# Performance work log

Hardware: AMD Instinct MI355X
Metric: run time of the kernel (lower is better)

The kernel has to match this reference:

```python
import jax, jax.numpy as jnp
import numpy as np

D = 1024

def setup_inputs() -> dict:
    key = jax.random.key(0)
    ks = jax.random.split(key, 9)
    s = 1.0 / np.sqrt(D)
    return {
        "x": jax.random.normal(ks[0], (4, 2048, D), dtype=jnp.float32),
        "y": jax.random.normal(ks[1], (4, 2048, D), dtype=jnp.float32),
        "z": jax.random.normal(ks[2], (4, 2048, D), dtype=jnp.float32),
        "Wq": jax.random.uniform(ks[3], (D, D), jnp.float32, -s, s),
        "bq": jax.random.uniform(ks[4], (D,), jnp.float32, -s, s),
        "Wk": jax.random.uniform(ks[5], (D, D), jnp.float32, -s, s),
        "bk": jax.random.uniform(ks[6], (D,), jnp.float32, -s, s),
        "Wv": jax.random.uniform(ks[7], (D, D), jnp.float32, -s, s),
        "bv": jax.random.uniform(ks[8], (D,), jnp.float32, -s, s),
    }

def reference(x, y, z, Wq, bq, Wk, bk, Wv, bv):
    # nn.Linear: x @ W^T + b
    Q = jnp.einsum('bsd,ed->bse', x, Wq) + bq  # [B,S,D]
    K = jnp.einsum('bsd,ed->bse', y, Wk) + bk
    V = jnp.einsum('bsd,ed->bse', z, Wv) + bv
    scores = jnp.einsum('bqd,bkd->bqk', Q, K) / jnp.sqrt(jnp.float32(Q.shape[-1]))
    weights = jax.nn.softmax(scores, axis=-1)  # [B,S,S]
    return jnp.einsum('bqk,bkd->bqd', weights, V)
```

## Files before the change

kernel.cpp:

```cpp
#include <hip/hip_runtime.h>
#include <hip/hip_bf16.h>

typedef unsigned short u16;
typedef __bf16 bf16x8 __attribute__((ext_vector_type(8)));
typedef float  f32x4  __attribute__((ext_vector_type(4)));
typedef u16    u16x8  __attribute__((ext_vector_type(8)));

__device__ __forceinline__ u16 f2bf(float f) {
    unsigned u = __float_as_uint(f);
    u = (u + 0x7fffu + ((u >> 16) & 1u)) >> 16;
    return (u16)u;
}
__device__ __forceinline__ float bf2f(u16 h) {
    return __uint_as_float(((unsigned)h) << 16);
}

__global__ __launch_bounds__(256) void cvt_bf16_kernel(
    const float* __restrict__ src, u16* __restrict__ dst, int n8)
{
    int i = blockIdx.x * 256 + threadIdx.x;
    if (i >= n8) return;
    const float4* s4 = (const float4*)src;
    float4 a = s4[2 * i], b = s4[2 * i + 1];
    u16x8 o;
    o[0] = f2bf(a.x); o[1] = f2bf(a.y); o[2] = f2bf(a.z); o[3] = f2bf(a.w);
    o[4] = f2bf(b.x); o[5] = f2bf(b.y); o[6] = f2bf(b.z); o[7] = f2bf(b.w);
    ((u16x8*)dst)[i] = o;
}

#define BMM 256
#define BNN 128
#define BKK 64
#define BUFU 24576
#define LDSB (3 * BUFU * 2)

__device__ __forceinline__ void gload_lds16(const void* g, void* l) {
    __builtin_amdgcn_global_load_lds(
        (__attribute__((address_space(1))) void*)g,
        (__attribute__((address_space(3))) void*)l, 16, 0, 0);
}

template<bool OUT_BF16, bool HAS_BIAS>
__global__ __launch_bounds__(512, 2) void gemm8p(
    const u16* __restrict__ A, const u16* __restrict__ Bm,
    const float* __restrict__ bias, void* __restrict__ C,
    int M, int N, int K, float scale,
    long long aBS, long long bBS, long long cBS)
{
    extern __shared__ u16 lds[];
    A  += (size_t)blockIdx.z * aBS;
    Bm += (size_t)blockIdx.z * bBS;

    const int m0 = blockIdx.y * BMM;
    const int n0 = blockIdx.x * BNN;
    const int tid  = threadIdx.x;
    const int lane = tid & 63;
    const int wave = tid >> 6;
    const int wm   = wave >> 2;
    const int wn   = wave & 3;
    const int fr   = lane & 15;
    const int kg   = lane >> 4;

    const int sl_a = lane >> 3;
    const int swsl = (lane & 7) ^ sl_a;
    const u16* gAs = A  + (size_t)(m0 + wave * 8 + sl_a) * K + swsl * 8;
    const u16* gBs = Bm + (size_t)(n0 + wave * 8 + sl_a) * K + swsl * 8;
    const int ldsW = wave * 512;

    auto stageA = [&](u16* wbase, size_t gc, int i) {
        gload_lds16(gAs + gc + (size_t)i * 64 * K, wbase + i * 4096 + ldsW);
    };
    auto stageB = [&](u16* wbase, size_t gc, int i) {
        gload_lds16(gBs + gc + (size_t)i * 64 * K, wbase + 16384 + i * 4096 + ldsW);
    };

    f32x4 acc[8][2] = {};

    const int NT = K / BKK;
    const int swz = fr & 7;

    {
        u16* b0 = lds;
        u16* b1 = lds + BUFU;
        #pragma unroll
        for (int i = 0; i < 4; ++i) stageA(b0, 0, i);
        #pragma unroll
        for (int i = 0; i < 2; ++i) stageB(b0, 0, i);
        #pragma unroll
        for (int i = 0; i < 4; ++i) stageA(b1, BKK, i);
        #pragma unroll
        for (int i = 0; i < 2; ++i) stageB(b1, BKK, i);
        asm volatile("s_waitcnt vmcnt(6)" ::: "memory");
        __builtin_amdgcn_s_barrier();
    }

    int br = 0, bw = 2;
    for (int t = 0; t < NT; ++t) {
        const u16* sa = lds + br * BUFU;
        const u16* sb = sa + 16384;
        u16* wbase = lds + bw * BUFU;
        const bool st = (t + 2 < NT);
        const size_t gc = (size_t)(t + 2) * BKK;

        bf16x8 bF[2][2];
        #pragma unroll
        for (int n = 0; n < 2; ++n)
            #pragma unroll
            for (int ks = 0; ks < 2; ++ks)
                bF[n][ks] = *(const bf16x8*)&sb[(wn * 32 + n * 16 + fr) * 64
                                + ((((ks << 2) | kg) ^ swz) << 3)];
        bf16x8 aF0[4][2];
        #pragma unroll
        for (int m = 0; m < 4; ++m)
            #pragma unroll
            for (int ks = 0; ks < 2; ++ks)
                aF0[m][ks] = *(const bf16x8*)&sa[(wm * 128 + m * 16 + fr) * 64
                                + ((((ks << 2) | kg) ^ swz) << 3)];
        if (st) { stageA(wbase, gc, 0); stageA(wbase, gc, 1); stageB(wbase, gc, 0); }
        __builtin_amdgcn_s_barrier();
        __builtin_amdgcn_s_setprio(1);
        #pragma unroll
        for (int m = 0; m < 4; ++m)
            #pragma unroll
            for (int n = 0; n < 2; ++n)
                #pragma unroll
                for (int ks = 0; ks < 2; ++ks)
                    acc[m][n] = __builtin_amdgcn_mfma_f32_16x16x32_bf16(
                        aF0[m][ks], bF[n][ks], acc[m][n], 0, 0, 0);
        __builtin_amdgcn_s_setprio(0);
        __builtin_amdgcn_s_barrier();

        bf16x8 aF1[4][2];
        #pragma unroll
        for (int m = 0; m < 4; ++m)
            #pragma unroll
            for (int ks = 0; ks < 2; ++ks)
                aF1[m][ks] = *(const bf16x8*)&sa[(wm * 128 + 64 + m * 16 + fr) * 64
                                + ((((ks << 2) | kg) ^ swz) << 3)];
        if (st) { stageA(wbase, gc, 2); stageA(wbase, gc, 3); stageB(wbase, gc, 1); }
        if (st) asm volatile("s_waitcnt vmcnt(6)" ::: "memory");
        else    asm volatile("s_waitcnt vmcnt(0)" ::: "memory");
        __builtin_amdgcn_s_barrier();
        __builtin_amdgcn_s_setprio(1);
        #pragma unroll
        for (int m = 0; m < 4; ++m)
            #pragma unroll
            for (int n = 0; n < 2; ++n)
                #pragma unroll
                for (int ks = 0; ks < 2; ++ks)
                    acc[4 + m][n] = __builtin_amdgcn_mfma_f32_16x16x32_bf16(
                        aF1[m][ks], bF[n][ks], acc[4 + m][n], 0, 0, 0);
        __builtin_amdgcn_s_setprio(0);
        __builtin_amdgcn_s_barrier();

        br = (br == 2) ? 0 : br + 1;
        bw = (bw == 2) ? 0 : bw + 1;
    }

    if (OUT_BF16) {
        u16* Cb = (u16*)C + (size_t)blockIdx.z * cBS;
        #pragma unroll
        for (int mi = 0; mi < 8; ++mi) {
            const int row0 = m0 + wm * 128 + mi * 16 + kg * 4;
            #pragma unroll
            for (int n = 0; n < 2; ++n) {
                const int col = n0 + wn * 32 + n * 16 + fr;
                const float badd = HAS_BIAS ? bias[col] : 0.0f;
                f32x4 v = acc[mi][n];
                #pragma unroll
                for (int q = 0; q < 4; ++q)
                    Cb[(size_t)(row0 + q) * N + col] = f2bf(v[q] * scale + badd);
            }
        }
    } else {
        float* Cf = (float*)C + (size_t)blockIdx.z * cBS;
        #pragma unroll
        for (int mi = 0; mi < 8; ++mi) {
            const int row0 = m0 + wm * 128 + mi * 16 + kg * 4;
            #pragma unroll
            for (int n = 0; n < 2; ++n) {
                const int col = n0 + wn * 32 + n * 16 + fr;
                const float badd = HAS_BIAS ? bias[col] : 0.0f;
                f32x4 v = acc[mi][n];
                #pragma unroll
                for (int q = 0; q < 4; ++q)
                    Cf[(size_t)(row0 + q) * N + col] = v[q] * scale + badd;
            }
        }
    }
}

__global__ __launch_bounds__(256) void transpose_bf16(
    const u16* __restrict__ V, u16* __restrict__ Vt)
{
    __shared__ u16 tile[64][72];
    const int b  = blockIdx.z;
    const int k0 = blockIdx.y * 64;
    const int d0 = blockIdx.x * 64;
    const int tr = threadIdx.x >> 3;
    const int tc = (threadIdx.x & 7) * 8;

    const u16* src = V + ((size_t)b * 2048 + k0) * 1024 + d0;
    #pragma unroll
    for (int i = 0; i < 2; ++i) {
        int r = tr + i * 32;
        *(u16x8*)&tile[r][tc] = *(const u16x8*)&src[(size_t)r * 1024 + tc];
    }
    __syncthreads();
    u16* dst = Vt + ((size_t)b * 1024 + d0) * 2048 + k0;
    #pragma unroll
    for (int i = 0; i < 2; ++i) {
        int r = tr + i * 32;
        u16x8 o;
        #pragma unroll
        for (int j = 0; j < 8; ++j) o[j] = tile[tc + j][r];
        *(u16x8*)&dst[(size_t)r * 2048 + tc] = o;
    }
}

__global__ __launch_bounds__(256) void softmax_kernel(u16* __restrict__ SP)
{
    const size_t row = blockIdx.x;
    u16x8* rp = (u16x8*)(SP + row * 2048);
    const int tid  = threadIdx.x;
    const int lane = tid & 63;
    const int wv   = tid >> 6;

    u16x8 v = rp[tid];
    float f[8];
    #pragma unroll
    for (int j = 0; j < 8; ++j) f[j] = bf2f(v[j]);

    float m = f[0];
    #pragma unroll
    for (int j = 1; j < 8; ++j) m = fmaxf(m, f[j]);
    #pragma unroll
    for (int o = 32; o; o >>= 1) m = fmaxf(m, __shfl_xor(m, o, 64));

    __shared__ float red[8];
    if (lane == 0) red[wv] = m;
    __syncthreads();
    m = fmaxf(fmaxf(red[0], red[1]), fmaxf(red[2], red[3]));

    float e[8], s = 0.f;
    #pragma unroll
    for (int j = 0; j < 8; ++j) { e[j] = __expf(f[j] - m); s += e[j]; }
    #pragma unroll
    for (int o = 32; o; o >>= 1) s += __shfl_xor(s, o, 64);
    if (lane == 0) red[4 + wv] = s;
    __syncthreads();
    s = (red[4] + red[5]) + (red[6] + red[7]);
    const float inv = 1.0f / s;

    u16x8 o8;
    #pragma unroll
    for (int j = 0; j < 8; ++j) o8[j] = f2bf(e[j] * inv);
    rp[tid] = o8;
}

extern "C" void kernel_launch(void* const* d_in, const int* in_sizes, int n_in,
                              void* d_out, int out_size, void* d_ws, size_t ws_size,
                              hipStream_t stream)
{
    const int Bn = 4, S = 2048, D = 1024;
    const size_t nx = (size_t)Bn * S * D;
    const size_t nw = (size_t)D * D;

    const float* x  = (const float*)d_in[0];
    const float* y  = (const float*)d_in[1];
    const float* z  = (const float*)d_in[2];
    const float* Wq = (const float*)d_in[3];
    const float* bq = (const float*)d_in[4];
    const float* Wk = (const float*)d_in[5];
    const float* bk = (const float*)d_in[6];
    const float* Wv = (const float*)d_in[7];
    const float* bv = (const float*)d_in[8];

    u16* xb  = (u16*)d_ws;
    u16* yb  = xb + nx;
    u16* zb  = yb + nx;
    u16* wqb = zb + nx;
    u16* wkb = wqb + nw;
    u16* wvb = wkb + nw;
    u16* Qb  = wvb + nw;
    u16* Kb  = Qb + nx;
    u16* Vb  = Kb + nx;
    u16* Vt  = Vb + nx;
    u16* Pb  = xb;

    hipFuncSetAttribute((const void*)gemm8p<true,  true >,
                        hipFuncAttributeMaxDynamicSharedMemorySize, LDSB);
    hipFuncSetAttribute((const void*)gemm8p<true,  false>,
                        hipFuncAttributeMaxDynamicSharedMemorySize, LDSB);
    hipFuncSetAttribute((const void*)gemm8p<false, false>,
                        hipFuncAttributeMaxDynamicSharedMemorySize, LDSB);

    const int n8x = (int)(nx / 8), n8w = (int)(nw / 8);
    cvt_bf16_kernel<<<(n8x + 255) / 256, 256, 0, stream>>>(x, xb, n8x);
    cvt_bf16_kernel<<<(n8x + 255) / 256, 256, 0, stream>>>(y, yb, n8x);
    cvt_bf16_kernel<<<(n8x + 255) / 256, 256, 0, stream>>>(z, zb, n8x);
    cvt_bf16_kernel<<<(n8w + 255) / 256, 256, 0, stream>>>(Wq, wqb, n8w);
    cvt_bf16_kernel<<<(n8w + 255) / 256, 256, 0, stream>>>(Wk, wkb, n8w);
    cvt_bf16_kernel<<<(n8w + 255) / 256, 256, 0, stream>>>(Wv, wvb, n8w);

    dim3 gQKV(D / BNN, (Bn * S) / BMM, 1);
    gemm8p<true, true><<<gQKV, 512, LDSB, stream>>>(xb, wqb, bq, Qb, Bn * S, D, D, 1.0f, 0, 0, 0);
    gemm8p<true, true><<<gQKV, 512, LDSB, stream>>>(yb, wkb, bk, Kb, Bn * S, D, D, 1.0f, 0, 0, 0);
    gemm8p<true, true><<<gQKV, 512, LDSB, stream>>>(zb, wvb, bv, Vb, Bn * S, D, D, 1.0f, 0, 0, 0);

    transpose_bf16<<<dim3(D / 64, S / 64, Bn), 256, 0, stream>>>(Vb, Vt);

    gemm8p<true, false><<<dim3(S / BNN, S / BMM, Bn), 512, LDSB, stream>>>(
        Qb, Kb, nullptr, Pb, S, S, D, 0.03125f,
        (long long)S * D, (long long)S * D, (long long)S * S);

    softmax_kernel<<<Bn * S, 256, 0, stream>>>(Pb);

    gemm8p<false, false><<<dim3(D / BNN, S / BMM, Bn), 512, LDSB, stream>>>(
        Pb, Vt, nullptr, d_out, S, D, S, 1.0f,
        (long long)S * S, (long long)D * S, (long long)S * D);
}
```

Before: 352.0 us.

## Reshape wave tiles to 64x64 and software-pipeline LDS fragment reads with fewer barriers

Each of the eight waves in the GEMM now computes a square 64x64 sub-tile in a 4x2 wave grid, replacing the 128x32 sub-tile in a 2x4 grid. Each MFMA batch then needs the same number of A and B fragment reads. The k-loop splits into two k-halves. The fragments for the next half are read from LDS while the current half's MFMAs run. All global-to-LDS staging for stage t+2 is issued at once, and only one barrier per iteration remains instead of four. The aim is more fragment reuse per LDS read and less synchronisation stall, at the cost of a hand-scheduled pipeline that relies on the waitcnt and barrier placement being exactly right.

```diff
diff --git a/kernel.cpp b/kernel.cpp
--- a/kernel.cpp
+++ b/kernel.cpp
@@ -28,11 +28,8 @@
     ((u16x8*)dst)[i] = o;
 }
 
-#define BMM 256
-#define BNN 128
-#define BKK 64
-#define BUFU 24576
-#define LDSB (3 * BUFU * 2)
+#define BUF_N 24576
+#define LDS_N (3 * BUF_N * 2)
 
 __device__ __forceinline__ void gload_lds16(const void* g, void* l) {
     __builtin_amdgcn_global_load_lds(
@@ -41,7 +38,7 @@
 }
 
 template<bool OUT_BF16, bool HAS_BIAS>
-__global__ __launch_bounds__(512, 2) void gemm8p(
+__global__ __launch_bounds__(512, 2) void gemm_p(
     const u16* __restrict__ A, const u16* __restrict__ Bm,
     const float* __restrict__ bias, void* __restrict__ C,
     int M, int N, int K, float scale,
@@ -51,122 +48,120 @@
     A  += (size_t)blockIdx.z * aBS;
     Bm += (size_t)blockIdx.z * bBS;
 
-    const int m0 = blockIdx.y * BMM;
-    const int n0 = blockIdx.x * BNN;
+    const int m0 = blockIdx.y * 256;
+    const int n0 = blockIdx.x * 128;
     const int tid  = threadIdx.x;
     const int lane = tid & 63;
     const int wave = tid >> 6;
-    const int wm   = wave >> 2;
-    const int wn   = wave & 3;
+    const int wm   = wave >> 1;
+    const int wn   = wave & 1;
     const int fr   = lane & 15;
     const int kg   = lane >> 4;
 
-    const int sl_a = lane >> 3;
-    const int swsl = (lane & 7) ^ sl_a;
-    const u16* gAs = A  + (size_t)(m0 + wave * 8 + sl_a) * K + swsl * 8;
-    const u16* gBs = Bm + (size_t)(n0 + wave * 8 + sl_a) * K + swsl * 8;
+    const int rl  = tid >> 3;
+    const int sw8 = ((tid & 7) ^ (rl & 7)) * 8;
+    const u16* gA = A  + (size_t)(m0 + rl) * K + sw8;
+    const u16* gB = Bm + (size_t)(n0 + rl) * K + sw8;
     const int ldsW = wave * 512;
 
-    auto stageA = [&](u16* wbase, size_t gc, int i) {
-        gload_lds16(gAs + gc + (size_t)i * 64 * K, wbase + i * 4096 + ldsW);
+    auto stA = [&](u16* bufb, int tk, int c) {
+        gload_lds16(gA + (size_t)c * 64 * K + (size_t)tk * 64,
+                    bufb + c * 4096 + ldsW);
     };
-    auto stageB = [&](u16* wbase, size_t gc, int i) {
-        gload_lds16(gBs + gc + (size_t)i * 64 * K, wbase + 16384 + i * 4096 + ldsW);
+    auto stB = [&](u16* bufb, int tk, int c) {
+        gload_lds16(gB + (size_t)c * 64 * K + (size_t)tk * 64,
+                    bufb + 16384 + c * 4096 + ldsW);
     };
 
-    f32x4 acc[8][2] = {};
-
-    const int NT = K / BKK;
-    const int swz = fr & 7;
-
-    {
-        u16* b0 = lds;
-        u16* b1 = lds + BUFU;
-        #pragma unroll
-        for (int i = 0; i < 4; ++i) stageA(b0, 0, i);
-        #pragma unroll
-        for (int i = 0; i < 2; ++i) stageB(b0, 0, i);
-        #pragma unroll
-        for (int i = 0; i < 4; ++i) stageA(b1, BKK, i);
-        #pragma unroll
-        for (int i = 0; i < 2; ++i) stageB(b1, BKK, i);
-        asm volatile("s_waitcnt vmcnt(6)" ::: "memory");
-        __builtin_amdgcn_s_barrier();
-    }
-
-    int br = 0, bw = 2;
+    auto rdA = [&](const u16* sa, int m, int ks) {
+        return *(const bf16x8*)&sa[(wm * 64 + m * 16 + fr) * 64
+                                   + ((((ks << 2) | kg) ^ (fr & 7)) << 3)];
+    };
+    auto rdB = [&](const u16* sb, int n, int ks) {
+        return *(const bf16x8*)&sb[(wn * 64 + n * 16 + fr) * 64
+                                   + ((((ks << 2) | kg) ^ (fr & 7)) << 3)];
+    };
+
+    f32x4 acc[4][4] = {};
+    bf16x8 a0[4], b0[4], a1[4], b1[4];
+    const int NT = K / 64;
+
+    u16 *p0 = lds, *p1 = lds + BUF_N, *p2 = lds + 2 * BUF_N;
+
+    #pragma unroll
+    for (int c = 0; c < 4; ++c) stA(p0, 0, c);
+    #pragma unroll
+    for (int c = 0; c < 2; ++c) stB(p0, 0, c);
+    #pragma unroll
+    for (int c = 0; c < 4; ++c) stA(p1, 1, c);
+    #pragma unroll
+    for (int c = 0; c < 2; ++c) stB(p1, 1, c);
+    asm volatile("s_waitcnt vmcnt(6)" ::: "memory");
+    __builtin_amdgcn_s_barrier();
+
+    #pragma unroll
+    for (int m = 0; m < 4; ++m) a0[m] = rdA(p0, m, 0);
+    #pragma unroll
+    for (int n = 0; n < 4; ++n) b0[n] = rdB(p0 + 16384, n, 0);
+
     for (int t = 0; t < NT; ++t) {
-        const u16* sa = lds + br * BUFU;
-        const u16* sb = sa + 16384;
-        u16* wbase = lds + bw * BUFU;
+        const u16* sa = p0;
+        const u16* sb = p0 + 16384;
         const bool st = (t + 2 < NT);
-        const size_t gc = (size_t)(t + 2) * BKK;
-
-        bf16x8 bF[2][2];
-        #pragma unroll
-        for (int n = 0; n < 2; ++n)
-            #pragma unroll
-            for (int ks = 0; ks < 2; ++ks)
-                bF[n][ks] = *(const bf16x8*)&sb[(wn * 32 + n * 16 + fr) * 64
-                                + ((((ks << 2) | kg) ^ swz) << 3)];
-        bf16x8 aF0[4][2];
+
+        #pragma unroll
+        for (int m = 0; m < 4; ++m) a1[m] = rdA(sa, m, 1);
+        #pragma unroll
+        for (int n = 0; n < 4; ++n) b1[n] = rdB(sb, n, 1);
+        if (st) {
+            #pragma unroll
+            for (int c = 0; c < 4; ++c) stA(p2, t + 2, c);
+            #pragma unroll
+            for (int c = 0; c < 2; ++c) stB(p2, t + 2, c);
+        }
+        __builtin_amdgcn_s_setprio(1);
         #pragma unroll
         for (int m = 0; m < 4; ++m)
             #pragma unroll
-            for (int ks = 0; ks < 2; ++ks)
-                aF0[m][ks] = *(const bf16x8*)&sa[(wm * 128 + m * 16 + fr) * 64
-                                + ((((ks << 2) | kg) ^ swz) << 3)];
-        if (st) { stageA(wbase, gc, 0); stageA(wbase, gc, 1); stageB(wbase, gc, 0); }
-        __builtin_amdgcn_s_barrier();
-        __builtin_amdgcn_s_setprio(1);
-        #pragma unroll
-        for (int m = 0; m < 4; ++m)
-            #pragma unroll
-            for (int n = 0; n < 2; ++n)
-                #pragma unroll
-                for (int ks = 0; ks < 2; ++ks)
-                    acc[m][n] = __builtin_amdgcn_mfma_f32_16x16x32_bf16(
-                        aF0[m][ks], bF[n][ks], acc[m][n], 0, 0, 0);
+            for (int n = 0; n < 4; ++n)
+                acc[m][n] = __builtin_amdgcn_mfma_f32_16x16x32_bf16(
+                    a0[m], b0[n], acc[m][n], 0, 0, 0);
         __builtin_amdgcn_s_setprio(0);
-        __builtin_amdgcn_s_barrier();
-
-        bf16x8 aF1[4][2];
-        #pragma unroll
-        for (int m = 0; m < 4; ++m)
-            #pragma unroll
-            for (int ks = 0; ks < 2; ++ks)
-                aF1[m][ks] = *(const bf16x8*)&sa[(wm * 128 + 64 + m * 16 + fr) * 64
-                                + ((((ks << 2) | kg) ^ swz) << 3)];
-        if (st) { stageA(wbase, gc, 2); stageA(wbase, gc, 3); stageB(wbase, gc, 1); }
+
+        asm volatile("s_waitcnt lgkmcnt(0)" ::: "memory");
         if (st) asm volatile("s_waitcnt vmcnt(6)" ::: "memory");
         else    asm volatile("s_waitcnt vmcnt(0)" ::: "memory");
         __builtin_amdgcn_s_barrier();
+        if (t + 1 < NT) {
+            const u16* na = p1;
+            const u16* nb = p1 + 16384;
+            #pragma unroll
+            for (int m = 0; m < 4; ++m) a0[m] = rdA(na, m, 0);
+            #pragma unroll
+            for (int n = 0; n < 4; ++n) b0[n] = rdB(nb, n, 0);
+        }
         __builtin_amdgcn_s_setprio(1);
         #pragma unroll
         for (int m = 0; m < 4; ++m)
             #pragma unroll
-            for (int n = 0; n < 2; ++n)
-                #pragma unroll
-                for (int ks = 0; ks < 2; ++ks)
-                    acc[4 + m][n] = __builtin_amdgcn_mfma_f32_16x16x32_bf16(
-                        aF1[m][ks], bF[n][ks], acc[4 + m][n], 0, 0, 0);
+            for (int n = 0; n < 4; ++n)
+                acc[m][n] = __builtin_amdgcn_mfma_f32_16x16x32_bf16(
+                    a1[m], b1[n], acc[m][n], 0, 0, 0);
         __builtin_amdgcn_s_setprio(0);
-        __builtin_amdgcn_s_barrier();
-
-        br = (br == 2) ? 0 : br + 1;
-        bw = (bw == 2) ? 0 : bw + 1;
+
+        u16* tmp = p0; p0 = p1; p1 = p2; p2 = tmp;
     }
 
     if (OUT_BF16) {
         u16* Cb = (u16*)C + (size_t)blockIdx.z * cBS;
         #pragma unroll
-        for (int mi = 0; mi < 8; ++mi) {
-            const int row0 = m0 + wm * 128 + mi * 16 + kg * 4;
-            #pragma unroll
-            for (int n = 0; n < 2; ++n) {
-                const int col = n0 + wn * 32 + n * 16 + fr;
+        for (int m = 0; m < 4; ++m) {
+            const int row0 = m0 + wm * 64 + m * 16 + kg * 4;
+            #pragma unroll
+            for (int n = 0; n < 4; ++n) {
+                const int col = n0 + wn * 64 + n * 16 + fr;
                 const float badd = HAS_BIAS ? bias[col] : 0.0f;
-                f32x4 v = acc[mi][n];
+                f32x4 v = acc[m][n];
                 #pragma unroll
                 for (int q = 0; q < 4; ++q)
                     Cb[(size_t)(row0 + q) * N + col] = f2bf(v[q] * scale + badd);
@@ -175,13 +170,13 @@
     } else {
         float* Cf = (float*)C + (size_t)blockIdx.z * cBS;
         #pragma unroll
-        for (int mi = 0; mi < 8; ++mi) {
-            const int row0 = m0 + wm * 128 + mi * 16 + kg * 4;
-            #pragma unroll
-            for (int n = 0; n < 2; ++n) {
-                const int col = n0 + wn * 32 + n * 16 + fr;
+        for (int m = 0; m < 4; ++m) {
+            const int row0 = m0 + wm * 64 + m * 16 + kg * 4;
+            #pragma unroll
+            for (int n = 0; n < 4; ++n) {
+                const int col = n0 + wn * 64 + n * 16 + fr;
                 const float badd = HAS_BIAS ? bias[col] : 0.0f;
-                f32x4 v = acc[mi][n];
+                f32x4 v = acc[m][n];
                 #pragma unroll
                 for (int q = 0; q < 4; ++q)
                     Cf[(size_t)(row0 + q) * N + col] = v[q] * scale + badd;
@@ -288,12 +283,12 @@
     u16* Vt  = Vb + nx;
     u16* Pb  = xb;
 
-    hipFuncSetAttribute((const void*)gemm8p<true,  true >,
-                        hipFuncAttributeMaxDynamicSharedMemorySize, LDSB);
-    hipFuncSetAttribute((const void*)gemm8p<true,  false>,
-                        hipFuncAttributeMaxDynamicSharedMemorySize, LDSB);
-    hipFuncSetAttribute((const void*)gemm8p<false, false>,
-                        hipFuncAttributeMaxDynamicSharedMemorySize, LDSB);
+    hipFuncSetAttribute((const void*)gemm_p<true,  true >,
+                        hipFuncAttributeMaxDynamicSharedMemorySize, LDS_N);
+    hipFuncSetAttribute((const void*)gemm_p<true,  false>,
+                        hipFuncAttributeMaxDynamicSharedMemorySize, LDS_N);
+    hipFuncSetAttribute((const void*)gemm_p<false, false>,
+                        hipFuncAttributeMaxDynamicSharedMemorySize, LDS_N);
 
     const int n8x = (int)(nx / 8), n8w = (int)(nw / 8);
     cvt_bf16_kernel<<<(n8x + 255) / 256, 256, 0, stream>>>(x, xb, n8x);
@@ -303,20 +298,20 @@
     cvt_bf16_kernel<<<(n8w + 255) / 256, 256, 0, stream>>>(Wk, wkb, n8w);
     cvt_bf16_kernel<<<(n8w + 255) / 256, 256, 0, stream>>>(Wv, wvb, n8w);
 
-    dim3 gQKV(D / BNN, (Bn * S) / BMM, 1);
-    gemm8p<true, true><<<gQKV, 512, LDSB, stream>>>(xb, wqb, bq, Qb, Bn * S, D, D, 1.0f, 0, 0, 0);
-    gemm8p<true, true><<<gQKV, 512, LDSB, stream>>>(yb, wkb, bk, Kb, Bn * S, D, D, 1.0f, 0, 0, 0);
-    gemm8p<true, true><<<gQKV, 512, LDSB, stream>>>(zb, wvb, bv, Vb, Bn * S, D, D, 1.0f, 0, 0, 0);
+    dim3 gQKV(D / 128, (Bn * S) / 256, 1);
+    gemm_p<true, true><<<gQKV, 512, LDS_N, stream>>>(xb, wqb, bq, Qb, Bn * S, D, D, 1.0f, 0, 0, 0);
+    gemm_p<true, true><<<gQKV, 512, LDS_N, stream>>>(yb, wkb, bk, Kb, Bn * S, D, D, 1.0f, 0, 0, 0);
+    gemm_p<true, true><<<gQKV, 512, LDS_N, stream>>>(zb, wvb, bv, Vb, Bn * S, D, D, 1.0f, 0, 0, 0);
 
     transpose_bf16<<<dim3(D / 64, S / 64, Bn), 256, 0, stream>>>(Vb, Vt);
 
-    gemm8p<true, false><<<dim3(S / BNN, S / BMM, Bn), 512, LDSB, stream>>>(
+    gemm_p<true, false><<<dim3(S / 128, S / 256, Bn), 512, LDS_N, stream>>>(
         Qb, Kb, nullptr, Pb, S, S, D, 0.03125f,
         (long long)S * D, (long long)S * D, (long long)S * S);
 
     softmax_kernel<<<Bn * S, 256, 0, stream>>>(Pb);
 
-    gemm8p<false, false><<<dim3(D / BNN, S / BMM, Bn), 512, LDSB, stream>>>(
+    gemm_p<false, false><<<dim3(D / 128, S / 256, Bn), 512, LDS_N, stream>>>(
         Pb, Vt, nullptr, d_out, S, D, S, 1.0f,
         (long long)S * S, (long long)D * S, (long long)S * D);
 }
```

Result: no change. 346.4 us (-1.6%).
